# Kernel optimization log

Hardware: AMD Instinct MI355X
Metric: run time of the kernel (lower is better)

## Reference

```python
import jax, jax.numpy as jnp
import numpy as np

OUT_H, OUT_W, GRID_SIZE = 256, 192, 5
N = GRID_SIZE * GRID_SIZE
BATCH = 64


def _make_constants():
    ax = np.linspace(-1.0, 1.0, GRID_SIZE)
    P_Y, P_X = np.meshgrid(ax, ax)
    P_X = P_X.reshape(-1).astype(np.float64)  # (N,)
    P_Y = P_Y.reshape(-1).astype(np.float64)
    d2 = (P_X[:, None] - P_X[None, :]) ** 2 + (P_Y[:, None] - P_Y[None, :]) ** 2
    d2[d2 == 0] = 1.0
    K = d2 * np.log(d2)
    P = np.stack([np.ones(N), P_X, P_Y], axis=1)  # (N,3)
    L = np.block([[K, P], [P.T, np.zeros((3, 3))]])  # (N+3, N+3)
    Li = np.linalg.inv(L).astype(np.float32)
    grid_X, grid_Y = np.meshgrid(np.linspace(-1, 1, OUT_W), np.linspace(-1, 1, OUT_H))
    return (P_X.astype(np.float32), P_Y.astype(np.float32), Li,
            grid_X.astype(np.float32), grid_Y.astype(np.float32))


_PX, _PY, _LI, _GX, _GY = _make_constants()


def setup_inputs() -> dict:
    key = jax.random.key(0)
    theta = jax.random.normal(key, (BATCH, 2 * N), dtype=jnp.float32) * 0.1
    return {"theta": theta}


def reference(theta) -> jnp.ndarray:
    P_X = jnp.asarray(_PX)          # (N,)
    P_Y = jnp.asarray(_PY)
    Li = jnp.asarray(_LI)           # (N+3, N+3)
    grid_X = jnp.asarray(_GX)       # (H, W)
    grid_Y = jnp.asarray(_GY)

    # Absolute control-point targets
    Q_X = theta[:, :N] + P_X        # (B, N)
    Q_Y = theta[:, N:] + P_Y

    # TPS coefficients: non-affine W (B,N) and affine A (B,3)
    W_X = jnp.einsum('nm,bm->bn', Li[:N, :N], Q_X)
    W_Y = jnp.einsum('nm,bm->bn', Li[:N, :N], Q_Y)
    A_X = jnp.einsum('km,bm->bk', Li[N:, :N], Q_X)  # (B,3): [c, cx, cy]
    A_Y = jnp.einsum('km,bm->bk', Li[N:, :N], Q_Y)

    # RBF kernel U(r^2) = r^2 log(r^2), evaluated per pixel per control point
    d2 = (grid_X[:, :, None] - P_X) ** 2 + (grid_Y[:, :, None] - P_Y) ** 2  # (H,W,N)
    d2 = jnp.where(d2 == 0, jnp.float32(1.0), d2)
    U = d2 * jnp.log(d2)            # (H,W,N)

    rbf_X = jnp.einsum('hwn,bn->bhw', U, W_X)
    rbf_Y = jnp.einsum('hwn,bn->bhw', U, W_Y)

    px = (A_X[:, 0, None, None] + A_X[:, 1, None, None] * grid_X
          + A_X[:, 2, None, None] * grid_Y + rbf_X)  # (B,H,W)
    py = (A_Y[:, 0, None, None] + A_Y[:, 1, None, None] * grid_X
          + A_Y[:, 2, None, None] * grid_Y + rbf_Y)

    return jnp.stack([px, py], axis=3)  # (B,H,W,2)
```

## Files before the change

kernel.cpp:

```cpp
#include <hip/hip_runtime.h>

#define OUT_H 256
#define OUT_W 192
#define HWPIX (OUT_H * OUT_W)
#define NPTS 25
#define BATCH 64


constexpr double cx_ln(double x) {
  int e = 0;
  while (x >= 1.5) { x *= 0.5; ++e; }
  while (x < 0.75) { x *= 2.0; --e; }
  double t = (x - 1.0) / (x + 1.0);
  double t2 = t * t, s = 0.0, term = t;
  for (int k = 0; k < 20; ++k) { s += term / (double)(2 * k + 1); term *= t2; }
  return 2.0 * s + (double)e * 0.6931471805599453094172321214581766;
}

struct Consts { float li[28][25]; };

constexpr Consts make_consts() {
  Consts out{};
  double PX[25] = {}, PY[25] = {};
  for (int n = 0; n < 25; ++n) {
    PX[n] = -1.0 + 0.5 * (double)(n / 5);
    PY[n] = -1.0 + 0.5 * (double)(n % 5);
  }
  double M[28][56] = {};
  for (int i = 0; i < 28; ++i)
    for (int j = 0; j < 56; ++j) M[i][j] = 0.0;
  for (int i = 0; i < 25; ++i) {
    for (int j = 0; j < 25; ++j) {
      double dx = PX[i] - PX[j], dy = PY[i] - PY[j];
      double d2 = dx * dx + dy * dy;
      M[i][j] = (d2 == 0.0) ? 0.0 : d2 * cx_ln(d2);
    }
    M[i][25] = 1.0; M[i][26] = PX[i]; M[i][27] = PY[i];
    M[25][i] = 1.0; M[26][i] = PX[i]; M[27][i] = PY[i];
  }
  for (int i = 0; i < 28; ++i) M[i][28 + i] = 1.0;
  for (int k = 0; k < 28; ++k) {
    int piv = k;
    double mx = M[k][k] < 0.0 ? -M[k][k] : M[k][k];
    for (int r = k + 1; r < 28; ++r) {
      double a = M[r][k] < 0.0 ? -M[r][k] : M[r][k];
      if (a > mx) { mx = a; piv = r; }
    }
    if (piv != k)
      for (int j = 0; j < 56; ++j) { double t = M[k][j]; M[k][j] = M[piv][j]; M[piv][j] = t; }
    double inv = 1.0 / M[k][k];
    for (int j = 0; j < 56; ++j) M[k][j] *= inv;
    for (int r = 0; r < 28; ++r) {
      if (r == k) continue;
      double f = M[r][k];
      if (f != 0.0)
        for (int j = 0; j < 56; ++j) M[r][j] -= f * M[k][j];
    }
  }
  for (int k = 0; k < 28; ++k)
    for (int m = 0; m < 25; ++m) out.li[k][m] = (float)M[k][28 + m];
  return out;
}

constexpr Consts CC = make_consts();

__device__ constexpr float PXf[25] = {
  -1.f,-1.f,-1.f,-1.f,-1.f, -0.5f,-0.5f,-0.5f,-0.5f,-0.5f,
   0.f, 0.f, 0.f, 0.f, 0.f,  0.5f, 0.5f, 0.5f, 0.5f, 0.5f,
   1.f, 1.f, 1.f, 1.f, 1.f };
__device__ constexpr float PYf[25] = {
  -1.f,-0.5f,0.f,0.5f,1.f, -1.f,-0.5f,0.f,0.5f,1.f,
  -1.f,-0.5f,0.f,0.5f,1.f, -1.f,-0.5f,0.f,0.5f,1.f,
  -1.f,-0.5f,0.f,0.5f,1.f };


__global__ __launch_bounds__(256) void tps_prep(const float* __restrict__ theta,
                                                float* __restrict__ C) {
  int t = threadIdx.x;
  for (int o = t; o < 3584; o += 256) {
    int b = o / 56, rem = o % 56;
    int axis = rem / 28, kk = rem % 28;
    const float* th = theta + b * 50 + axis * 25;
    float acc = 0.f;
#pragma unroll
    for (int m = 0; m < 25; ++m) {
      float pv = axis ? PYf[m] : PXf[m];
      acc += CC.li[kk][m] * (th[m] + pv);
    }
    C[o] = acc;
  }
}


__global__ __launch_bounds__(256) void tps_main(const float* __restrict__ C,
                                                float2* __restrict__ out) {
  int lane = threadIdx.x & 63;
  int wg = __builtin_amdgcn_readfirstlane((int)(threadIdx.x >> 6));
  int p = (blockIdx.x << 6) + lane;
  int w = p % OUT_W;
  int h = p / OUT_W;
  float gx = (float)(-1.0 + (double)w * (2.0 / 191.0));
  float gy = (float)(-1.0 + (double)h * (2.0 / 255.0));
  if (w == OUT_W - 1) gx = 1.0f;
  if (h == OUT_H - 1) gy = 1.0f;

  float U[28];
#pragma unroll
  for (int n = 0; n < 25; ++n) {
    float dx = gx - PXf[n];
    float dy = gy - PYf[n];
    float d2 = dx * dx + dy * dy;
    float u = d2 * __logf(d2);
    U[n] = (d2 == 0.0f) ? 0.0f : u;
  }
  U[25] = 1.0f; U[26] = gx; U[27] = gy;

  const float* Cw = C + wg * 16 * 56;
  for (int i = 0; i < 16; ++i) {
    const float* Cb = Cw + i * 56;
    float px = 0.f, py = 0.f;
#pragma unroll
    for (int k = 0; k < 28; ++k) {
      px += U[k] * Cb[k];
      py += U[k] * Cb[28 + k];
    }
    int b = (wg << 4) + i;
    out[b * HWPIX + p] = make_float2(px, py);
  }
}


extern "C" void kernel_launch(void* const* d_in, const int* in_sizes, int n_in,
                              void* d_out, int out_size, void* d_ws, size_t ws_size,
                              hipStream_t stream) {
  const float* theta = (const float*)d_in[0];
  float* C = (float*)d_ws;
  float2* out = (float2*)d_out;

  hipLaunchKernelGGL(tps_prep, dim3(1), dim3(256), 0, stream, theta, C);
  hipLaunchKernelGGL(tps_main, dim3(HWPIX / 64), dim3(256), 0, stream, C, out);
}
```

Before: 80.09 us.

## Fuse TPS coefficient prep into main kernel with per-block shared-memory coefficients

Removes the single-block prep kernel and its launch. Every block of the main kernel now loads theta into shared memory and recomputes all 64x56 TPS coefficients itself, with the P_X/P_Y contribution folded into constant offsets at compile time. Coefficients are stored interleaved (x,y) in LDS so the main loop reads them as float4. This trades a serial single-block prologue and a kernel boundary for redundant per-block compute and extra LDS use, about 27 KB per block.

```diff
diff --git a/kernel.cpp b/kernel.cpp
--- a/kernel.cpp
+++ b/kernel.cpp
@@ -3,7 +3,6 @@
 #define OUT_H 256
 #define OUT_W 192
 #define HWPIX (OUT_H * OUT_W)
-#define NPTS 25
 #define BATCH 64
 
 
@@ -17,7 +16,10 @@
   return 2.0 * s + (double)e * 0.6931471805599453094172321214581766;
 }
 
-struct Consts { float li[28][25]; };
+struct Consts {
+  float li[28][25];
+  float cp[2][28];
+};
 
 constexpr Consts make_consts() {
   Consts out{};
@@ -59,6 +61,13 @@
   }
   for (int k = 0; k < 28; ++k)
     for (int m = 0; m < 25; ++m) out.li[k][m] = (float)M[k][28 + m];
+  for (int axis = 0; axis < 2; ++axis)
+    for (int k = 0; k < 28; ++k) {
+      double s = 0.0;
+      for (int m = 0; m < 25; ++m)
+        s += (double)out.li[k][m] * (axis ? PY[m] : PX[m]);
+      out.cp[axis][k] = (float)s;
+    }
   return out;
 }
 
@@ -74,31 +83,47 @@
   -1.f,-0.5f,0.f,0.5f,1.f };
 
 
-__global__ __launch_bounds__(256) void tps_prep(const float* __restrict__ theta,
-                                                float* __restrict__ C) {
-  int t = threadIdx.x;
-  for (int o = t; o < 3584; o += 256) {
-    int b = o / 56, rem = o % 56;
-    int axis = rem / 28, kk = rem % 28;
-    const float* th = theta + b * 50 + axis * 25;
-    float acc = 0.f;
+__global__ __launch_bounds__(256) void tps_fused(const float* __restrict__ theta,
+                                                 float2* __restrict__ out) {
+  __shared__ float sth[BATCH * 50];
+  __shared__ float sC[BATCH * 56];
+  const int t = threadIdx.x;
+
+  {
+    const float4* g4 = (const float4*)theta;
+    float4* s4 = (float4*)sth;
 #pragma unroll
-    for (int m = 0; m < 25; ++m) {
-      float pv = axis ? PYf[m] : PXf[m];
-      acc += CC.li[kk][m] * (th[m] + pv);
+    for (int i = 0; i < 4; ++i) {
+      int idx = t + i * 256;
+      if (idx < 800) s4[idx] = g4[idx];
     }
-    C[o] = acc;
   }
-}
+  __syncthreads();
 
+  {
+    const int pair = t & 127;
+    const int b = pair >> 1, axis = pair & 1;
+    const int kg = t >> 7;
+    float th[25];
+    const float* src = sth + b * 50 + axis * 25;
+#pragma unroll
+    for (int m = 0; m < 25; ++m) th[m] = src[m];
+#pragma unroll
+    for (int j = 0; j < 14; ++j) {
+      const int k = kg * 14 + j;
+      float acc = CC.cp[axis][k];
+#pragma unroll
+      for (int m = 0; m < 25; ++m) acc += CC.li[k][m] * th[m];
+      sC[b * 56 + k * 2 + axis] = acc;
+    }
+  }
+  __syncthreads();
 
-__global__ __launch_bounds__(256) void tps_main(const float* __restrict__ C,
-                                                float2* __restrict__ out) {
-  int lane = threadIdx.x & 63;
-  int wg = __builtin_amdgcn_readfirstlane((int)(threadIdx.x >> 6));
-  int p = (blockIdx.x << 6) + lane;
-  int w = p % OUT_W;
-  int h = p / OUT_W;
+  const int lane = t & 63;
+  const int wg = t >> 6;
+  const int p = (blockIdx.x << 6) + lane;
+  const int w = p % OUT_W;
+  const int h = p / OUT_W;
   float gx = (float)(-1.0 + (double)w * (2.0 / 191.0));
   float gy = (float)(-1.0 + (double)h * (2.0 / 255.0));
   if (w == OUT_W - 1) gx = 1.0f;
@@ -115,17 +140,19 @@
   }
   U[25] = 1.0f; U[26] = gx; U[27] = gy;
 
-  const float* Cw = C + wg * 16 * 56;
+  const float4* cb = (const float4*)sC + wg * 16 * 14;
+  float2* op = out + p;
+#pragma unroll 4
   for (int i = 0; i < 16; ++i) {
-    const float* Cb = Cw + i * 56;
+    const float4* c4 = cb + i * 14;
     float px = 0.f, py = 0.f;
 #pragma unroll
-    for (int k = 0; k < 28; ++k) {
-      px += U[k] * Cb[k];
-      py += U[k] * Cb[28 + k];
+    for (int j = 0; j < 14; ++j) {
+      float4 c = c4[j];
+      px += U[2 * j]     * c.x;  py += U[2 * j]     * c.y;
+      px += U[2 * j + 1] * c.z;  py += U[2 * j + 1] * c.w;
     }
-    int b = (wg << 4) + i;
-    out[b * HWPIX + p] = make_float2(px, py);
+    op[(wg * 16 + i) * HWPIX] = make_float2(px, py);
   }
 }
 
@@ -134,9 +161,6 @@
                               void* d_out, int out_size, void* d_ws, size_t ws_size,
                               hipStream_t stream) {
   const float* theta = (const float*)d_in[0];
-  float* C = (float*)d_ws;
   float2* out = (float2*)d_out;
-
-  hipLaunchKernelGGL(tps_prep, dim3(1), dim3(256), 0, stream, theta, C);
-  hipLaunchKernelGGL(tps_main, dim3(HWPIX / 64), dim3(256), 0, stream, C, out);
+  hipLaunchKernelGGL(tps_fused, dim3(HWPIX / 64), dim3(256), 0, stream, theta, out);
 }
```

Result: faster. 75.19 us (-6.1%).
